# Performance work log

Hardware: AMD Instinct MI355X
Metric: run time of the kernel (lower is better)

The kernel has to match this reference:

```python
import jax, jax.numpy as jnp
import numpy as np

N = 50000      # nodes
M = 800000     # edges
D = 128        # node_state_dim == msg_dim
EF = 32        # edge_feat_dim
DF = 32        # node_dist_feat_dim
ATT = 128      # att_hidden_dim
L = 2          # num_layer (num_prop = 1)
IN = D + EF + DF  # 192, MLP input dim


def setup_inputs() -> dict:
    key = jax.random.key(0)
    ks = jax.random.split(key, 18)
    rn = lambda k, shape, s=0.05: jax.random.normal(k, shape, dtype=jnp.float32) * s
    return {
        "node_feat":   rn(ks[0], (N, D), 1.0),
        "node_feat_c": rn(ks[1], (N, D), 1.0),
        "edge":        jax.random.randint(ks[2], (M, 2), 0, N, dtype=jnp.int32),
        "edge_feat":   rn(ks[3], (M, EF), 1.0),
        "dist_feat":   rn(ks[4], (M, DF), 1.0),
        # msg MLP: Linear(IN->D) -> ReLU -> Linear(D->D), stacked over layers
        "msg_w0": rn(ks[5], (L, IN, D)),  "msg_b0": jnp.zeros((L, D), jnp.float32),
        "msg_w1": rn(ks[6], (L, D, D)),   "msg_b1": jnp.zeros((L, D), jnp.float32),
        # attention head: Linear(IN->ATT) -> ReLU -> Linear(ATT->D) -> Sigmoid
        "att_w0": rn(ks[7], (L, IN, ATT)), "att_b0": jnp.zeros((L, ATT), jnp.float32),
        "att_w1": rn(ks[8], (L, ATT, D)),  "att_b1": jnp.zeros((L, D), jnp.float32),
        # LSTMCell params (torch layout: W_ih [4H, in], W_hh [4H, H], gate order i,f,g,o)
        "lstm_wih": rn(ks[9],  (L, 4 * D, D)),
        "lstm_whh": rn(ks[10], (L, 4 * D, D)),
        "lstm_bih": jnp.zeros((L, 4 * D), jnp.float32),
        "lstm_bhh": jnp.zeros((L, 4 * D), jnp.float32),
    }


def _lstm_cell(x, h, c, wih, whh, bih, bhh):
    gates = x @ wih.T + bih + h @ whh.T + bhh          # [N, 4D]
    i, f, g, o = jnp.split(gates, 4, axis=1)
    c2 = jax.nn.sigmoid(f) * c + jax.nn.sigmoid(i) * jnp.tanh(g)
    h2 = jax.nn.sigmoid(o) * jnp.tanh(c2)
    return h2, c2


def reference(node_feat, node_feat_c, edge, edge_feat, dist_feat,
              msg_w0, msg_b0, msg_w1, msg_b1,
              att_w0, att_b0, att_w1, att_b1,
              lstm_wih, lstm_whh, lstm_bih, lstm_bhh):
    src = edge[:, 0]
    dst = edge[:, 1]
    state, state_c = node_feat, node_feat_c
    for ii in range(L):
        if ii > 0:
            state = jax.nn.relu(state)
        # _prop (num_prop = 1)
        state_diff = state[src] - state[dst]                               # [M, D]
        edge_input = jnp.concatenate([state_diff, edge_feat, dist_feat], 1)  # [M, IN]
        msg = jax.nn.relu(edge_input @ msg_w0[ii] + msg_b0[ii]) @ msg_w1[ii] + msg_b1[ii]
        att = jax.nn.sigmoid(
            jax.nn.relu(edge_input @ att_w0[ii] + att_b0[ii]) @ att_w1[ii] + att_b1[ii])
        msg = msg * att
        state_msg = jax.ops.segment_sum(msg, dst, num_segments=N)          # scatter_add
        state, state_c = _lstm_cell(state_msg, state, state_c,
                                    lstm_wih[ii], lstm_whh[ii],
                                    lstm_bih[ii], lstm_bhh[ii])
    return state
```

## Files before the change

### kernel.cpp

```cpp
#include <hip/hip_runtime.h>
#include <hip/hip_bf16.h>

constexpr int N  = 50000;
constexpr int M  = 800000;
constexpr int D  = 128;
constexpr int IN = 192;
constexpr int TE = 128;
constexpr int NCH = 20;
constexpr int NBLK = (N + 255) / 256;

typedef __attribute__((ext_vector_type(4)))  short short4v;
typedef __attribute__((ext_vector_type(8)))  short short8;
typedef __attribute__((ext_vector_type(16))) float f32x16;
typedef _Float16 half8  __attribute__((ext_vector_type(8)));

__device__ __align__(16) short g_wp[163840];
__device__ __align__(16) short g_lw[262144];
__device__ __align__(16) short g_efdf[(size_t)M * 64];
__device__ __align__(16) short g_sbf[(size_t)N * D];
__device__ int g_cnt[N];
__device__ int g_part[NBLK];
__device__ int g_ssrc[M];
__device__ int g_sdst[M];
__device__ int g_inv[M];

__device__ __forceinline__ float sigm(float x) { return 1.0f / (1.0f + __expf(-x)); }

__device__ __forceinline__ void barrier_lgkm() {
    asm volatile("s_waitcnt lgkmcnt(0)" ::: "memory");
    __builtin_amdgcn_s_barrier();
}

__device__ __forceinline__ short f2bf(float f) {
    unsigned u = __builtin_bit_cast(unsigned, f);
    u = (u + 0x7FFFu + ((u >> 16) & 1u)) >> 16;
    return (short)u;
}
__device__ __forceinline__ unsigned pk2(float a, float b) {
    __hip_bfloat162 h = __float22bfloat162_rn(float2{a, b});
    unsigned u;
    __builtin_memcpy(&u, &h, 4);
    return u;
}
__device__ __forceinline__ unsigned pkh(float a, float b) {
    auto h = __builtin_amdgcn_cvt_pkrtz(a, b);
    unsigned u;
    __builtin_memcpy(&u, &h, 4);
    return u;
}
__device__ __forceinline__ short f2h(float f) {
    _Float16 h = (_Float16)f;
    return __builtin_bit_cast(short, h);
}
__device__ __forceinline__ float h2f(short s) {
    _Float16 h = __builtin_bit_cast(_Float16, s);
    return (float)h;
}

__global__ void zero_cnt_kernel() {
    for (int i = blockIdx.x * 256 + threadIdx.x; i < N; i += gridDim.x * 256) g_cnt[i] = 0;
}
__global__ void hist_kernel(const int* __restrict__ edge) {
    int e = blockIdx.x * 256 + threadIdx.x;
    if (e < M) atomicAdd(&g_cnt[edge[e * 2 + 1]], 1);
}
__global__ void scanA_kernel() {
    __shared__ int red[256];
    const int t = threadIdx.x;
    const int idx = blockIdx.x * 256 + t;
    red[t] = (idx < N) ? g_cnt[idx] : 0;
    __syncthreads();
#pragma unroll
    for (int s = 128; s > 0; s >>= 1) {
        if (t < s) red[t] += red[t + s];
        __syncthreads();
    }
    if (t == 0) g_part[blockIdx.x] = red[0];
}
__global__ void scanB_kernel() {
    __shared__ int sh[256];
    const int t = threadIdx.x;
    int v = (t < NBLK) ? g_part[t] : 0;
    sh[t] = v;
    __syncthreads();
    int x = v;
    for (int s = 1; s < 256; s <<= 1) {
        int y = (t >= s) ? sh[t - s] : 0;
        __syncthreads();
        x += y; sh[t] = x;
        __syncthreads();
    }
    if (t < NBLK) g_part[t] = x - v;
}
__global__ void scanC_kernel() {
    __shared__ int sh[256];
    const int t = threadIdx.x;
    const int idx = blockIdx.x * 256 + t;
    int v = (idx < N) ? g_cnt[idx] : 0;
    sh[t] = v;
    __syncthreads();
    int x = v;
    for (int s = 1; s < 256; s <<= 1) {
        int y = (t >= s) ? sh[t - s] : 0;
        __syncthreads();
        x += y; sh[t] = x;
        __syncthreads();
    }
    if (idx < N) g_cnt[idx] = g_part[blockIdx.x] + x - v;
}
__global__ void scatter_kernel(const int* __restrict__ edge) {
    int e = blockIdx.x * 256 + threadIdx.x;
    if (e < M) {
        const int s = edge[e * 2], d = edge[e * 2 + 1];
        const int p = atomicAdd(&g_cnt[d], 1);
        g_ssrc[p] = s;
        g_sdst[p] = d;
        g_inv[p]  = e;
    }
}

__global__ void pack_edge(const float* __restrict__ w0m, const float* __restrict__ w0a,
                          const float* __restrict__ w1m, const float* __restrict__ w1a) {
    int gid = blockIdx.x * 256 + threadIdx.x;
    int ii = gid / 81920;
    int r  = gid % 81920;
    int p  = r / 40960;  r %= 40960;
    int which = (r >= 24576) ? 1 : 0;
    int r2 = which ? r - 24576 : r;
    int e    = r2 & 7;
    int f    = r2 >> 3;
    int lane = f & 63;
    int ktct = f >> 6;
    int ct = ktct & 3, kt = ktct >> 2;
    int k   = kt * 16 + ((lane >> 5) << 3) + e;
    int col = ct * 32 + (lane & 31);
    const float* w0 = p ? w0a : w0m;
    const float* w1 = p ? w1a : w1m;
    float v = which ? w1[((size_t)ii * D + k) * D + col]
                    : w0[((size_t)ii * IN + k) * D + col];
    g_wp[gid] = f2h(v);
}

__global__ void pack_lstm(const float* __restrict__ wih, const float* __restrict__ whh) {
    int gid = blockIdx.x * 256 + threadIdx.x;
    int ii = gid >> 17;
    int r  = gid & 131071;
    int e = r & 7, f = r >> 3;
    int lane = f & 63, rest = f >> 6;
    int cf = rest & 15, kt = rest >> 4;
    int col = cf * 32 + (lane & 31);
    int k   = (kt & 7) * 16 + ((lane >> 5) << 3) + e;
    const float* src = (kt < 8) ? wih : whh;
    g_lw[gid] = f2bf(src[((size_t)ii * 512 + col) * D + k]);
}

__global__ void pack_efdf(const float* __restrict__ ef, const float* __restrict__ df) {
    int gid = blockIdx.x * 256 + threadIdx.x;
    int p = gid >> 3, c0 = (gid & 7) * 8;
    const int e = g_inv[p];
    const float* s = (c0 < 32) ? (ef + (size_t)e * 32 + c0) : (df + (size_t)e * 32 + (c0 - 32));
    float4 u0 = *(const float4*)s, u1 = *(const float4*)(s + 4);
    short8 t;
    unsigned* tp = (unsigned*)&t;
    tp[0] = pkh(u0.x, u0.y); tp[1] = pkh(u0.z, u0.w);
    tp[2] = pkh(u1.x, u1.y); tp[3] = pkh(u1.z, u1.w);
    *(short8*)(g_efdf + (size_t)gid * 8) = t;
}

__global__ void init_kernel(const float4* __restrict__ nf, const float4* __restrict__ nfc,
                            float4* __restrict__ state, float4* __restrict__ state_c,
                            float4* __restrict__ msg) {
    const int total = N * D / 4;
    const float4 z = make_float4(0.f, 0.f, 0.f, 0.f);
    for (int i = blockIdx.x * blockDim.x + threadIdx.x; i < total; i += gridDim.x * blockDim.x) {
        float4 v = nf[i];
        state[i]   = v;
        state_c[i] = nfc[i];
        short4v b;
        unsigned* bp = (unsigned*)&b;
        bp[0] = pkh(v.x, v.y); bp[1] = pkh(v.z, v.w);
        *(short4v*)(g_sbf + (size_t)i * 4) = b;
        msg[i] = z;
    }
}

#define MFMA16(a, b, c) __builtin_amdgcn_mfma_f32_32x32x16_f16(a, b, c, 0, 0, 0)
#define MFMABF(a, b, c) __builtin_amdgcn_mfma_f32_32x32x16_bf16(a, b, c, 0, 0, 0)

template<int BASE, int NC, bool FROM_H>
__device__ __forceinline__ void gemm_phase(const short8* __restrict__ gsrc, short8* wb,
                                           short8& gA, const half8 a1[12],
                                           const short (*hsr)[136],
                                           int tid, int lane, int cg, int half,
                                           f32x16& o0, f32x16& o1) {
    f32x16 acc0 = {}, acc1 = {};
#pragma unroll
    for (int c = 0; c < NC; ++c) {
        const int gc = BASE + c;
        short8 gB;
        if (gc + 2 < NCH) gB = gsrc[(size_t)(gc + 2) * 512 + tid];
        const short8* buf = wb + (gc & 1) * 512;
#pragma unroll
        for (int kl = 0; kl < 2; ++kl) {
            const int kt = c * 2 + kl;
            half8 a = FROM_H
                ? __builtin_bit_cast(half8, *(const short8*)&hsr[lane & 31][kt * 16 + half])
                : a1[kt];
            half8 b0 = __builtin_bit_cast(half8, buf[(kl * 4 + cg * 2 + 0) * 64 + lane]);
            half8 b1 = __builtin_bit_cast(half8, buf[(kl * 4 + cg * 2 + 1) * 64 + lane]);
            acc0 = MFMA16(a, b0, acc0);
            acc1 = MFMA16(a, b1, acc1);
        }
        if (gc + 1 < NCH) wb[((gc + 1) & 1) * 512 + tid] = gA;
        barrier_lgkm();
        if (gc + 2 < NCH) gA = gB;
    }
    o0 = acc0; o1 = acc1;
}

__device__ __forceinline__ void hwrite(short (*hsr)[136], const f32x16& a0, const f32x16& a1v,
                                       const float* __restrict__ b0, int lane, int cg) {
#pragma unroll
    for (int ct = 0; ct < 2; ++ct) {
        const int col = cg * 64 + ct * 32 + (lane & 31);
        const float bv = b0[col];
        f32x16 a = ct ? a1v : a0;
#pragma unroll
        for (int rp = 0; rp < 8; ++rp) {
            const int reg = rp * 2;
            const int row = (reg & 3) + 8 * (reg >> 2) + 4 * (lane >> 5);
            const unsigned pr = pkh(fmaxf(a[reg] + bv, 0.f), fmaxf(a[reg + 1] + bv, 0.f));
            hsr[row][col]     = (short)(pr & 0xFFFF);
            hsr[row + 1][col] = (short)(pr >> 16);
        }
    }
}

__global__ __launch_bounds__(512, 4)
void edge_mfma(int ii,
               const float* __restrict__ b0m, const float* __restrict__ b1m,
               const float* __restrict__ b0a, const float* __restrict__ b1a,
               float* __restrict__ state_msg) {
    __shared__ __align__(16) char pool[51712];
    short8* wb = (short8*)pool;
    short (*hs)[32][136] = (short(*)[32][136])(pool + 16384);
    int* sdst = (int*)(pool + 51200);

    const int tid  = threadIdx.x;
    const int lane = tid & 63;
    const int w    = tid >> 6;
    const int rt   = w >> 1;
    const int cg   = w & 1;
    const int e0   = blockIdx.x * TE;

    if (tid < TE) sdst[tid] = g_sdst[e0 + tid];

    const int er   = e0 + rt * 32 + (lane & 31);
    const int half = (lane >> 5) << 3;
    const int s  = g_ssrc[er];
    const int d2 = g_sdst[er];
    const short* srow = g_sbf + (size_t)s  * D;
    const short* drow = g_sbf + (size_t)d2 * D;
    half8 a1[12];
#pragma unroll
    for (int kt = 0; kt < 8; ++kt) {
        const int k0 = kt * 16 + half;
        half8 sv = __builtin_bit_cast(half8, *(const short8*)(srow + k0));
        half8 dv = __builtin_bit_cast(half8, *(const short8*)(drow + k0));
        a1[kt] = sv - dv;
    }
#pragma unroll
    for (int kt = 8; kt < 12; ++kt)
        a1[kt] = __builtin_bit_cast(half8, *(const short8*)(g_efdf + (size_t)er * 64 + (kt - 8) * 16 + half));

    const short8* gsrc = (const short8*)(g_wp + (size_t)ii * 81920);

    wb[tid] = gsrc[tid];
    short8 gA = gsrc[512 + tid];
    barrier_lgkm();

    f32x16 t0, t1, m0, m1, c0, c1;
    gemm_phase<0, 6, false>(gsrc, wb, gA, a1, hs[rt], tid, lane, cg, half, t0, t1);
    hwrite(hs[rt], t0, t1, b0m, lane, cg);
    barrier_lgkm();
    gemm_phase<6, 4, true>(gsrc, wb, gA, a1, hs[rt], tid, lane, cg, half, m0, m1);

    unsigned mb[16];
#pragma unroll
    for (int ct = 0; ct < 2; ++ct) {
        const float bm = b1m[cg * 64 + ct * 32 + (lane & 31)];
        f32x16 mv = ct ? m1 : m0;
#pragma unroll
        for (int rp = 0; rp < 8; ++rp)
            mb[ct * 8 + rp] = pkh(mv[rp * 2] + bm, mv[rp * 2 + 1] + bm);
    }

    gemm_phase<10, 6, false>(gsrc, wb, gA, a1, hs[rt], tid, lane, cg, half, t0, t1);
    hwrite(hs[rt], t0, t1, b0a, lane, cg);
    barrier_lgkm();
    gemm_phase<16, 4, true>(gsrc, wb, gA, a1, hs[rt], tid, lane, cg, half, c0, c1);

    float (*vt)[132] = (float(*)[132])pool;
    const int colr = tid & 127;
    const int sub  = tid >> 7;
#pragma unroll
    for (int pass = 0; pass < 2; ++pass) {
        if ((rt >> 1) == pass) {
#pragma unroll
            for (int ct = 0; ct < 2; ++ct) {
                const int col = cg * 64 + ct * 32 + (lane & 31);
                const float ba = b1a[col];
                f32x16 av = ct ? c1 : c0;
#pragma unroll
                for (int rp = 0; rp < 8; ++rp) {
                    const int reg = rp * 2;
                    const unsigned u = mb[ct * 8 + rp];
                    const int row = (rt & 1) * 32 + (reg & 3) + 8 * (reg >> 2) + 4 * (lane >> 5);
                    vt[row][col]     = h2f((short)(u & 0xFFFF)) * sigm(av[reg] + ba);
                    vt[row + 1][col] = h2f((short)(u >> 16))    * sigm(av[reg + 1] + ba);
                }
            }
        }
        barrier_lgkm();
        const int gbase = pass * 64 + sub * 16;
        float run = 0.f;
        int cur = sdst[gbase];
#pragma unroll 4
        for (int r = 0; r < 16; ++r) {
            const int dd = sdst[gbase + r];
            if (dd != cur) {
                atomicAdd(state_msg + (size_t)cur * D + colr, run);
                run = 0.f; cur = dd;
            }
            run += vt[sub * 16 + r][colr];
        }
        atomicAdd(state_msg + (size_t)cur * D + colr, run);
        barrier_lgkm();
    }
}

__global__ __launch_bounds__(256, 4)
void lstm_mfma(float* __restrict__ x, float* __restrict__ hbuf, float* __restrict__ cbuf,
               int ii, int last,
               const float* __restrict__ bih, const float* __restrict__ bhh) {
    __shared__ short8 wb[2048];
    const int tid  = threadIdx.x;
    const int lane = tid & 63;
    const int w    = tid >> 6;
    const int n0   = blockIdx.x * 32;
    const int half = (lane >> 5) << 3;
    const int nl   = lane & 31;
    const int nld  = min(n0 + nl, N - 1);

    const short8* gsrc = (const short8*)(g_lw + (size_t)ii * 131072);

    {
        short8 g[4];
#pragma unroll
        for (int i = 0; i < 4; ++i) g[i] = gsrc[tid + i * 256];
#pragma unroll
        for (int i = 0; i < 4; ++i) wb[tid + i * 256] = g[i];
        __syncthreads();
    }

    f32x16 acc[4] = {};
#pragma unroll
    for (int kt = 0; kt < 16; ++kt) {
        const float* srow = (kt < 8) ? (x + (size_t)nld * D + kt * 16 + half)
                                     : (hbuf + (size_t)nld * D + (kt - 8) * 16 + half);
        float4 u0 = *(const float4*)(srow);
        float4 u1 = *(const float4*)(srow + 4);
        short8 a;
        unsigned* ap = (unsigned*)&a;
        ap[0] = pk2(u0.x, u0.y); ap[1] = pk2(u0.z, u0.w);
        ap[2] = pk2(u1.x, u1.y); ap[3] = pk2(u1.z, u1.w);

        short8 g[4];
        if (kt + 1 < 16) {
            const short8* p = gsrc + (size_t)(kt + 1) * 1024;
#pragma unroll
            for (int i = 0; i < 4; ++i) g[i] = p[tid + i * 256];
        }
        const short8* buf = wb + (kt & 1) * 1024;
#pragma unroll
        for (int q = 0; q < 4; ++q) {
            short8 b = buf[(q * 4 + w) * 64 + lane];
            acc[q] = MFMABF(a, b, acc[q]);
        }
        if (kt + 1 < 16) {
            short8* d = wb + ((kt + 1) & 1) * 1024;
#pragma unroll
            for (int i = 0; i < 4; ++i) d[tid + i * 256] = g[i];
        }
        __syncthreads();
    }

    const int col = (w << 5) + nl;
    const float bi = bih[col]       + bhh[col];
    const float bf = bih[128 + col] + bhh[128 + col];
    const float bg = bih[256 + col] + bhh[256 + col];
    const float bo = bih[384 + col] + bhh[384 + col];
#pragma unroll
    for (int reg = 0; reg < 16; ++reg) {
        const int nn = (reg & 3) + 8 * (reg >> 2) + 4 * (lane >> 5);
        const int n = n0 + nn;
        if (n < N) {
            const float gi = acc[0][reg] + bi;
            const float gf = acc[1][reg] + bf;
            const float gg = acc[2][reg] + bg;
            const float go = acc[3][reg] + bo;
            float* cp = cbuf + (size_t)n * D + col;
            const float c2 = sigm(gf) * (*cp) + sigm(gi) * tanhf(gg);
            const float h2 = sigm(go) * tanhf(c2);
            *cp = c2;
            const float ho = last ? h2 : fmaxf(h2, 0.f);
            hbuf[(size_t)n * D + col] = ho;
            if (!last) g_sbf[(size_t)n * D + col] = f2h(ho);
        }
    }

    if (!last) {
        float4* xr = (float4*)(x + (size_t)n0 * D);
        const float4 z = make_float4(0.f, 0.f, 0.f, 0.f);
#pragma unroll
        for (int i = 0; i < 4; ++i) {
            const int idx = tid + i * 256;
            if (n0 + (idx >> 5) < N) xr[idx] = z;
        }
    }
}

extern "C" void kernel_launch(void* const* d_in, const int* in_sizes, int n_in,
                              void* d_out, int out_size, void* d_ws, size_t ws_size,
                              hipStream_t stream) {
    const float* node_feat   = (const float*)d_in[0];
    const float* node_feat_c = (const float*)d_in[1];
    const int*   edge        = (const int*)d_in[2];
    const float* edge_feat   = (const float*)d_in[3];
    const float* dist_feat   = (const float*)d_in[4];
    const float* msg_w0 = (const float*)d_in[5];
    const float* msg_b0 = (const float*)d_in[6];
    const float* msg_w1 = (const float*)d_in[7];
    const float* msg_b1 = (const float*)d_in[8];
    const float* att_w0 = (const float*)d_in[9];
    const float* att_b0 = (const float*)d_in[10];
    const float* att_w1 = (const float*)d_in[11];
    const float* att_b1 = (const float*)d_in[12];
    const float* lstm_wih = (const float*)d_in[13];
    const float* lstm_whh = (const float*)d_in[14];
    const float* lstm_bih = (const float*)d_in[15];
    const float* lstm_bhh = (const float*)d_in[16];

    float* state     = (float*)d_out;
    float* state_c   = (float*)d_ws;
    float* state_msg = (float*)d_ws + (size_t)N * D;

    zero_cnt_kernel<<<256, 256, 0, stream>>>();
    hist_kernel<<<(M + 255) / 256, 256, 0, stream>>>(edge);
    scanA_kernel<<<NBLK, 256, 0, stream>>>();
    scanB_kernel<<<1, 256, 0, stream>>>();
    scanC_kernel<<<NBLK, 256, 0, stream>>>();
    scatter_kernel<<<(M + 255) / 256, 256, 0, stream>>>(edge);

    pack_efdf<<<25000, 256, 0, stream>>>(edge_feat, dist_feat);
    pack_edge<<<640, 256, 0, stream>>>(msg_w0, att_w0, msg_w1, att_w1);
    pack_lstm<<<1024, 256, 0, stream>>>(lstm_wih, lstm_whh);

    init_kernel<<<2048, 256, 0, stream>>>((const float4*)node_feat, (const float4*)node_feat_c,
                                          (float4*)state, (float4*)state_c, (float4*)state_msg);

    for (int ii = 0; ii < 2; ++ii) {
        edge_mfma<<<M / TE, 512, 0, stream>>>(
            ii,
            msg_b0 + (size_t)ii * D, msg_b1 + (size_t)ii * D,
            att_b0 + (size_t)ii * D, att_b1 + (size_t)ii * D,
            state_msg);

        lstm_mfma<<<(N + 31) / 32, 256, 0, stream>>>(
            state_msg, state, state_c, ii, (ii == 1) ? 1 : 0,
            lstm_bih + (size_t)ii * 4 * D, lstm_bhh + (size_t)ii * 4 * D);
    }
}
```

Baseline: 855.8 us.

## Shrink edge tile to 64 edges with finer weight chunks and streamed edge features

```diff
diff --git a/kernel.cpp b/kernel.cpp
--- a/kernel.cpp
+++ b/kernel.cpp
@@ -5,8 +5,8 @@
 constexpr int M  = 800000;
 constexpr int D  = 128;
 constexpr int IN = 192;
-constexpr int TE = 128;
-constexpr int NCH = 20;
+constexpr int TE = 64;
+constexpr int NCH = 40;
 constexpr int NBLK = (N + 255) / 256;
 
 typedef __attribute__((ext_vector_type(4)))  short short4v;
@@ -187,38 +187,37 @@
 #define MFMA16(a, b, c) __builtin_amdgcn_mfma_f32_32x32x16_f16(a, b, c, 0, 0, 0)
 #define MFMABF(a, b, c) __builtin_amdgcn_mfma_f32_32x32x16_bf16(a, b, c, 0, 0, 0)
 
-template<int BASE, int NC, bool FROM_H>
+template<int BASE, int NC, int AMODE>
 __device__ __forceinline__ void gemm_phase(const short8* __restrict__ gsrc, short8* wb,
-                                           short8& gA, const half8 a1[12],
-                                           const short (*hsr)[136],
+                                           short8& gA, const half8* a1,
+                                           const short (*hsr)[132], const short* __restrict__ efrow,
                                            int tid, int lane, int cg, int half,
-                                           f32x16& o0, f32x16& o1) {
-    f32x16 acc0 = {}, acc1 = {};
+                                           f32x16& acc0, f32x16& acc1) {
+    short8 ef_cur, ef_nxt;
+    if (AMODE == 2) ef_cur = *(const short8*)(efrow);
 #pragma unroll
     for (int c = 0; c < NC; ++c) {
         const int gc = BASE + c;
         short8 gB;
-        if (gc + 2 < NCH) gB = gsrc[(size_t)(gc + 2) * 512 + tid];
-        const short8* buf = wb + (gc & 1) * 512;
-#pragma unroll
-        for (int kl = 0; kl < 2; ++kl) {
-            const int kt = c * 2 + kl;
-            half8 a = FROM_H
-                ? __builtin_bit_cast(half8, *(const short8*)&hsr[lane & 31][kt * 16 + half])
-                : a1[kt];
-            half8 b0 = __builtin_bit_cast(half8, buf[(kl * 4 + cg * 2 + 0) * 64 + lane]);
-            half8 b1 = __builtin_bit_cast(half8, buf[(kl * 4 + cg * 2 + 1) * 64 + lane]);
-            acc0 = MFMA16(a, b0, acc0);
-            acc1 = MFMA16(a, b1, acc1);
-        }
-        if (gc + 1 < NCH) wb[((gc + 1) & 1) * 512 + tid] = gA;
+        if (gc + 2 < NCH) gB = gsrc[(size_t)(gc + 2) * 256 + tid];
+        if (AMODE == 2 && c + 1 < NC) ef_nxt = *(const short8*)(efrow + (c + 1) * 16);
+        const short8* buf = wb + (gc & 1) * 256;
+        half8 a;
+        if (AMODE == 0)      a = a1[c];
+        else if (AMODE == 1) a = __builtin_bit_cast(half8, *(const short8*)&hsr[lane & 31][c * 16 + half]);
+        else                 a = __builtin_bit_cast(half8, ef_cur);
+        half8 b0 = __builtin_bit_cast(half8, buf[(cg * 2 + 0) * 64 + lane]);
+        half8 b1 = __builtin_bit_cast(half8, buf[(cg * 2 + 1) * 64 + lane]);
+        acc0 = MFMA16(a, b0, acc0);
+        acc1 = MFMA16(a, b1, acc1);
+        if (gc + 1 < NCH) wb[((gc + 1) & 1) * 256 + tid] = gA;
         barrier_lgkm();
         if (gc + 2 < NCH) gA = gB;
-    }
-    o0 = acc0; o1 = acc1;
-}
-
-__device__ __forceinline__ void hwrite(short (*hsr)[136], const f32x16& a0, const f32x16& a1v,
+        if (AMODE == 2) ef_cur = ef_nxt;
+    }
+}
+
+__device__ __forceinline__ void hwrite(short (*hsr)[132], const f32x16& a0, const f32x16& a1v,
                                        const float* __restrict__ b0, int lane, int cg) {
 #pragma unroll
     for (int ct = 0; ct < 2; ++ct) {
@@ -236,15 +235,15 @@
     }
 }
 
-__global__ __launch_bounds__(512, 4)
+__global__ __launch_bounds__(256, 5)
 void edge_mfma(int ii,
                const float* __restrict__ b0m, const float* __restrict__ b1m,
                const float* __restrict__ b0a, const float* __restrict__ b1a,
                float* __restrict__ state_msg) {
-    __shared__ __align__(16) char pool[51712];
+    __shared__ __align__(16) char pool[25344];
     short8* wb = (short8*)pool;
-    short (*hs)[32][136] = (short(*)[32][136])(pool + 16384);
-    int* sdst = (int*)(pool + 51200);
+    short (*hs)[32][132] = (short(*)[32][132])(pool + 8192);
+    int* sdst = (int*)(pool + 25088);
 
     const int tid  = threadIdx.x;
     const int lane = tid & 63;
@@ -269,21 +268,22 @@
         half8 dv = __builtin_bit_cast(half8, *(const short8*)(drow + k0));
         a1[kt] = sv - dv;
     }
+    const short* efrow = g_efdf + (size_t)er * 64 + half;
 #pragma unroll
     for (int kt = 8; kt < 12; ++kt)
-        a1[kt] = __builtin_bit_cast(half8, *(const short8*)(g_efdf + (size_t)er * 64 + (kt - 8) * 16 + half));
+        a1[kt] = __builtin_bit_cast(half8, *(const short8*)(efrow + (kt - 8) * 16));
 
     const short8* gsrc = (const short8*)(g_wp + (size_t)ii * 81920);
 
     wb[tid] = gsrc[tid];
-    short8 gA = gsrc[512 + tid];
+    short8 gA = gsrc[256 + tid];
     barrier_lgkm();
 
-    f32x16 t0, t1, m0, m1, c0, c1;
-    gemm_phase<0, 6, false>(gsrc, wb, gA, a1, hs[rt], tid, lane, cg, half, t0, t1);
+    f32x16 t0 = {}, t1 = {}, m0 = {}, m1 = {}, c0 = {}, c1 = {};
+    gemm_phase<0, 12, 0>(gsrc, wb, gA, a1, hs[rt], efrow, tid, lane, cg, half, t0, t1);
     hwrite(hs[rt], t0, t1, b0m, lane, cg);
     barrier_lgkm();
-    gemm_phase<6, 4, true>(gsrc, wb, gA, a1, hs[rt], tid, lane, cg, half, m0, m1);
+    gemm_phase<12, 8, 1>(gsrc, wb, gA, a1, hs[rt], efrow, tid, lane, cg, half, m0, m1);
 
     unsigned mb[16];
 #pragma unroll
@@ -295,17 +295,19 @@
             mb[ct * 8 + rp] = pkh(mv[rp * 2] + bm, mv[rp * 2 + 1] + bm);
     }
 
-    gemm_phase<10, 6, false>(gsrc, wb, gA, a1, hs[rt], tid, lane, cg, half, t0, t1);
+    t0 = (f32x16){}; t1 = (f32x16){};
+    gemm_phase<20, 8, 0>(gsrc, wb, gA, a1, hs[rt], efrow, tid, lane, cg, half, t0, t1);
+    gemm_phase<28, 4, 2>(gsrc, wb, gA, a1, hs[rt], efrow, tid, lane, cg, half, t0, t1);
     hwrite(hs[rt], t0, t1, b0a, lane, cg);
     barrier_lgkm();
-    gemm_phase<16, 4, true>(gsrc, wb, gA, a1, hs[rt], tid, lane, cg, half, c0, c1);
-
-    float (*vt)[132] = (float(*)[132])pool;
+    gemm_phase<32, 8, 1>(gsrc, wb, gA, a1, hs[rt], efrow, tid, lane, cg, half, c0, c1);
+
+    float (*vt)[132] = (float(*)[132])(pool + 8192);
     const int colr = tid & 127;
-    const int sub  = tid >> 7;
+    const int sub  = (tid >> 7) & 1;
 #pragma unroll
     for (int pass = 0; pass < 2; ++pass) {
-        if ((rt >> 1) == pass) {
+        if (rt == pass) {
 #pragma unroll
             for (int ct = 0; ct < 2; ++ct) {
                 const int col = cg * 64 + ct * 32 + (lane & 31);
@@ -315,14 +317,14 @@
                 for (int rp = 0; rp < 8; ++rp) {
                     const int reg = rp * 2;
                     const unsigned u = mb[ct * 8 + rp];
-                    const int row = (rt & 1) * 32 + (reg & 3) + 8 * (reg >> 2) + 4 * (lane >> 5);
+                    const int row = (reg & 3) + 8 * (reg >> 2) + 4 * (lane >> 5);
                     vt[row][col]     = h2f((short)(u & 0xFFFF)) * sigm(av[reg] + ba);
                     vt[row + 1][col] = h2f((short)(u >> 16))    * sigm(av[reg + 1] + ba);
                 }
             }
         }
         barrier_lgkm();
-        const int gbase = pass * 64 + sub * 16;
+        const int gbase = pass * 32 + sub * 16;
         float run = 0.f;
         int cur = sdst[gbase];
 #pragma unroll 4
@@ -470,7 +472,7 @@
                                           (float4*)state, (float4*)state_c, (float4*)state_msg);
 
     for (int ii = 0; ii < 2; ++ii) {
-        edge_mfma<<<M / TE, 512, 0, stream>>>(
+        edge_mfma<<<M / TE, 256, 0, stream>>>(
             ii,
             msg_b0 + (size_t)ii * D, msg_b1 + (size_t)ii * D,
             att_b0 + (size_t)ii * D, att_b1 + (size_t)ii * D,
```

Result: slower. 1.094 ms (+27.8%).
